# Kernel optimization log

Hardware: AMD Instinct MI355X
Metric: run time of the kernel (lower is better)

Reference implementation:

```python
import jax, jax.numpy as jnp
import numpy as np

T = 200000  # stack depth
V = 130     # vocab_size == input_dim
H = 512     # hid_dim
L = 2       # n_layers


def setup_inputs() -> dict:
    key = jax.random.key(0)
    ks = jax.random.split(key, 24)
    s = 0.05
    inp = {
        "input": jax.random.normal(ks[0], (1, 1, V), jnp.float32),
        "prev_Val": jax.random.normal(ks[1], (T, V), jnp.float32),
        "prev_stg": jax.random.uniform(ks[2], (T,), jnp.float32),
        "prev_read": jax.random.normal(ks[3], (V,), jnp.float32),
        "prev_h": jax.random.normal(ks[4], (L, 1, H), jnp.float32) * 0.1,
        "prev_c": jax.random.normal(ks[5], (L, 1, H), jnp.float32) * 0.1,
        # LSTM layer 0 (pytorch layout: W_ih (4H, in), W_hh (4H, H), gates i,f,g,o)
        "W_ih0": jax.random.normal(ks[6], (4 * H, V), jnp.float32) * s,
        "W_hh0": jax.random.normal(ks[7], (4 * H, H), jnp.float32) * s,
        "b_ih0": jax.random.normal(ks[8], (4 * H,), jnp.float32) * s,
        "b_hh0": jax.random.normal(ks[9], (4 * H,), jnp.float32) * s,
        # LSTM layer 1
        "W_ih1": jax.random.normal(ks[10], (4 * H, H), jnp.float32) * s,
        "W_hh1": jax.random.normal(ks[11], (4 * H, H), jnp.float32) * s,
        "b_ih1": jax.random.normal(ks[12], (4 * H,), jnp.float32) * s,
        "b_hh1": jax.random.normal(ks[13], (4 * H,), jnp.float32) * s,
        # gate heads (original inits these to zeros; random here to exercise math)
        "Wd": jax.random.normal(ks[14], (H,), jnp.float32) * s,
        "Bd": jax.random.normal(ks[15], (), jnp.float32) * s,
        "Wu": jax.random.normal(ks[16], (H,), jnp.float32) * s,
        "Bu": jax.random.normal(ks[17], (), jnp.float32) * s,
        "Wv": jax.random.normal(ks[18], (H, V), jnp.float32) * s,
        "Bv": jax.random.normal(ks[19], (V,), jnp.float32) * s,
        "Wo": jax.random.normal(ks[20], (H, H), jnp.float32) * s,
        "Bo": jax.random.normal(ks[21], (H,), jnp.float32) * s,
    }
    return inp


def _lstm_cell(x, h, c, Wih, Whh, bih, bhh):
    # x: (1, in), h/c: (1, H)
    g = x @ Wih.T + h @ Whh.T + bih + bhh  # (1, 4H)
    i, f, gg, o = jnp.split(g, 4, axis=-1)
    c2 = jax.nn.sigmoid(f) * c + jax.nn.sigmoid(i) * jnp.tanh(gg)
    h2 = jax.nn.sigmoid(o) * jnp.tanh(c2)
    return h2, c2


def reference(input, prev_Val, prev_stg, prev_read, prev_h, prev_c,
              W_ih0, W_hh0, b_ih0, b_hh0, W_ih1, W_hh1, b_ih1, b_hh1,
              Wd, Bd, Wu, Bu, Wv, Bv, Wo, Bo):
    x = (input + prev_read)[0]  # (1, V), seq_len == 1, batch == 1
    h1, c1 = _lstm_cell(x, prev_h[0], prev_c[0], W_ih0, W_hh0, b_ih0, b_hh0)
    h2, c2 = _lstm_cell(h1, prev_h[1], prev_c[1], W_ih1, W_hh1, b_ih1, b_hh1)
    output = h2  # (1, H)

    dt = jax.nn.sigmoid(output @ Wd + Bd)[0]      # scalar push strength
    ut = jax.nn.sigmoid(output @ Wu + Bu)[0]      # scalar pop strength
    vt = jnp.tanh(output @ Wv + Bv)               # (1, V) pushed value
    ot = jnp.tanh(output @ Wo + Bo)               # (1, H) controller output

    Val = jnp.concatenate([prev_Val, vt], axis=0)  # (T+1, V)

    # pop pass (top -> bottom): stg[i] = max(0, prev_stg[i] - max(0, ut)); ut -= stg[i]
    def pop_step(u, s):
        sn = jnp.maximum(0.0, s - jnp.maximum(0.0, u))
        return u - sn, sn
    _, stg_popped = jax.lax.scan(pop_step, ut, prev_stg, reverse=True)
    stg = jnp.concatenate([stg_popped, dt[None]])  # (T+1,)

    # read pass (top -> bottom): coef = min(stg[i], max(0, read)); read -= stg[i]
    def read_step(r, s):
        coef = jnp.minimum(s, jnp.maximum(0.0, r))
        return r - s, coef
    _, coefs = jax.lax.scan(read_step, jnp.asarray(1.0, stg.dtype), stg, reverse=True)
    rt = coefs @ Val  # (V,)

    h_new = jnp.stack([h1, h2])  # (L, 1, H)
    c_new = jnp.stack([c1, c2])
    return ot, Val, stg, rt, h_new, c_new
```

## Files before the change

kernel.cpp:

```cpp
#include <hip/hip_runtime.h>

#define T_DEPTH 200000
#define V_DIM   130
#define H_DIM   512

#define OT_OFF   0
#define VAL_OFF  512
#define STG_OFF  26000642
#define RT_OFF   26200643
#define HN_OFF   26200773
#define CN_OFF   26201797

#define WS_G0     0
#define WS_H1     2048
#define WS_C1     2560
#define WS_G1     3072
#define WS_H2     5120
#define WS_C2     5632
#define WS_VTACC  6144
#define WS_OTACC  6274
#define WS_DTUT   6786
#define WS_VT     6788
#define WS_TOTAL  6918

static __device__ __forceinline__ float sigmoidf(float x) {
    return 1.0f / (1.0f + expf(-x));
}

__global__ void k_bulk(const float4* __restrict__ val_in,
                       const float2* __restrict__ stg_in,
                       float* __restrict__ out) {
    const int NV4 = (T_DEPTH * V_DIM) / 4;
    const int NS2 = T_DEPTH / 2;
    const int NT  = NV4 + NS2;
    float4* __restrict__ val_out = reinterpret_cast<float4*>(out + VAL_OFF);
    float2* __restrict__ stg_out = reinterpret_cast<float2*>(out + STG_OFF);
    int stride = gridDim.x * blockDim.x;
    for (int u = blockIdx.x * blockDim.x + threadIdx.x; u < NT; u += stride) {
        if (u < NV4) {
            val_out[u] = val_in[u];
        } else {
            int s = u - NV4;
            stg_out[s] = stg_in[s];
        }
    }
}

__global__ void k_g0(const float* __restrict__ Wih, const float* __restrict__ Whh,
                     const float* __restrict__ bih, const float* __restrict__ bhh,
                     const float* __restrict__ inp, const float* __restrict__ prd,
                     const float* __restrict__ h0, float* __restrict__ g) {
    int wave = threadIdx.x >> 6, lane = threadIdx.x & 63;
    int row = blockIdx.x * 4 + wave;
    const float* wr = Wih + row * V_DIM;
    const float* wh = Whh + row * H_DIM;
    float p = 0.f;
    for (int c = lane; c < V_DIM; c += 64) p += wr[c] * (inp[c] + prd[c]);
    for (int k = lane; k < H_DIM; k += 64) p += wh[k] * h0[k];
    for (int off = 32; off; off >>= 1) p += __shfl_down(p, off, 64);
    if (lane == 0) g[row] = p + bih[row] + bhh[row];
}

__global__ void k_g1(const float* __restrict__ Wih, const float* __restrict__ Whh,
                     const float* __restrict__ bih, const float* __restrict__ bhh,
                     const float* __restrict__ h1, const float* __restrict__ hprev,
                     float* __restrict__ g) {
    int wave = threadIdx.x >> 6, lane = threadIdx.x & 63;
    int row = blockIdx.x * 4 + wave;
    const float* wr = Wih + row * H_DIM;
    const float* wh = Whh + row * H_DIM;
    float p = 0.f;
    for (int k = lane; k < H_DIM; k += 64) p += wr[k] * h1[k] + wh[k] * hprev[k];
    for (int off = 32; off; off >>= 1) p += __shfl_down(p, off, 64);
    if (lane == 0) g[row] = p + bih[row] + bhh[row];
}

__global__ void k_cell(const float* __restrict__ g, const float* __restrict__ cprev,
                       float* __restrict__ h, float* __restrict__ c,
                       float* __restrict__ h_out, float* __restrict__ c_out) {
    int j = threadIdx.x;
    float ig = sigmoidf(g[j]);
    float fg = sigmoidf(g[H_DIM + j]);
    float gg = tanhf(g[2 * H_DIM + j]);
    float og = sigmoidf(g[3 * H_DIM + j]);
    float cn = fg * cprev[j] + ig * gg;
    float hn = og * tanhf(cn);
    h[j] = hn; c[j] = cn;
    h_out[j] = hn;
    c_out[j] = cn;
}

__global__ void k_heads(const float* __restrict__ h2, const float* __restrict__ Wv,
                        const float* __restrict__ Wo, float* __restrict__ vt_acc,
                        float* __restrict__ ot_acc) {
    int t = threadIdx.x;
    int b = blockIdx.x;
    float a0 = 0.f, a1 = 0.f, av = 0.f;
    for (int kk = 0; kk < 16; ++kk) {
        int k = b * 16 + kk;
        float hv = h2[k];
        a0 += hv * Wo[k * H_DIM + t];
        a1 += hv * Wo[k * H_DIM + t + 256];
        if (t < V_DIM) av += hv * Wv[k * V_DIM + t];
    }
    atomicAdd(&ot_acc[t], a0);
    atomicAdd(&ot_acc[t + 256], a1);
    if (t < V_DIM) atomicAdd(&vt_acc[t], av);
}

__global__ void k_hfin(const float* __restrict__ h2,
                       const float* __restrict__ Wd, const float* __restrict__ Bd,
                       const float* __restrict__ Wu, const float* __restrict__ Bu,
                       const float* __restrict__ Bv, const float* __restrict__ Bo,
                       const float* __restrict__ vt_acc, const float* __restrict__ ot_acc,
                       float* __restrict__ dtut, float* __restrict__ vt,
                       float* __restrict__ out) {
    __shared__ float sd[H_DIM], su[H_DIM];
    int t = threadIdx.x;
    sd[t] = h2[t] * Wd[t];
    su[t] = h2[t] * Wu[t];
    __syncthreads();
    for (int s = 256; s; s >>= 1) {
        if (t < s) { sd[t] += sd[t + s]; su[t] += su[t + s]; }
        __syncthreads();
    }
    if (t == 0) {
        float dt = sigmoidf(sd[0] + Bd[0]);
        float ut = sigmoidf(su[0] + Bu[0]);
        dtut[0] = dt; dtut[1] = ut;
        out[STG_OFF + T_DEPTH] = dt;
    }
    float ot = tanhf(ot_acc[t] + Bo[t]);
    out[OT_OFF + t] = ot;
    if (t < V_DIM) {
        float v = tanhf(vt_acc[t] + Bv[t]);
        vt[t] = v;
        out[VAL_OFF + T_DEPTH * V_DIM + t] = v;
    }
}

__global__ void k_top(const float* __restrict__ prev_stg, const float* __restrict__ prev_val,
                      const float* __restrict__ dtut, const float* __restrict__ vt,
                      float* __restrict__ out) {
    int t = threadIdx.x;
    float dt = dtut[0];
    float u  = dtut[1];
    float r  = 1.0f;
    float acc = 0.f;
    {
        float coef = fminf(dt, fmaxf(0.f, r));
        if (t < V_DIM) acc += coef * vt[t];
        r -= dt;
    }
    for (int i = T_DEPTH - 1; i >= 0; --i) {
        bool pop_active = (u > 0.f);
        if (!pop_active && r <= 0.f) break;
        float s  = prev_stg[i];
        float sn = fmaxf(0.f, s - fmaxf(0.f, u));
        u -= sn;
        if (pop_active && t == 0) out[STG_OFF + i] = sn;
        float coef = fminf(sn, fmaxf(0.f, r));
        r -= sn;
        if (coef > 0.f && t < V_DIM) acc += coef * prev_val[i * V_DIM + t];
    }
    if (t < V_DIM) out[RT_OFF + t] = acc;
}

extern "C" void kernel_launch(void* const* d_in, const int* in_sizes, int n_in,
                              void* d_out, int out_size, void* d_ws, size_t ws_size,
                              hipStream_t stream) {
    (void)in_sizes; (void)n_in; (void)out_size; (void)ws_size;
    const float* input     = (const float*)d_in[0];
    const float* prev_Val  = (const float*)d_in[1];
    const float* prev_stg  = (const float*)d_in[2];
    const float* prev_read = (const float*)d_in[3];
    const float* prev_h    = (const float*)d_in[4];
    const float* prev_c    = (const float*)d_in[5];
    const float* W_ih0 = (const float*)d_in[6];
    const float* W_hh0 = (const float*)d_in[7];
    const float* b_ih0 = (const float*)d_in[8];
    const float* b_hh0 = (const float*)d_in[9];
    const float* W_ih1 = (const float*)d_in[10];
    const float* W_hh1 = (const float*)d_in[11];
    const float* b_ih1 = (const float*)d_in[12];
    const float* b_hh1 = (const float*)d_in[13];
    const float* Wd = (const float*)d_in[14];
    const float* Bd = (const float*)d_in[15];
    const float* Wu = (const float*)d_in[16];
    const float* Bu = (const float*)d_in[17];
    const float* Wv = (const float*)d_in[18];
    const float* Bv = (const float*)d_in[19];
    const float* Wo = (const float*)d_in[20];
    const float* Bo = (const float*)d_in[21];

    float* out = (float*)d_out;
    float* ws  = (float*)d_ws;

    hipMemsetAsync(d_ws, 0, WS_TOTAL * sizeof(float), stream);

    k_bulk<<<4096, 256, 0, stream>>>((const float4*)prev_Val, (const float2*)prev_stg, out);

    k_g0<<<512, 256, 0, stream>>>(W_ih0, W_hh0, b_ih0, b_hh0, input, prev_read,
                                  prev_h, ws + WS_G0);
    k_cell<<<1, 512, 0, stream>>>(ws + WS_G0, prev_c, ws + WS_H1, ws + WS_C1,
                                  out + HN_OFF, out + CN_OFF);
    k_g1<<<512, 256, 0, stream>>>(W_ih1, W_hh1, b_ih1, b_hh1, ws + WS_H1,
                                  prev_h + H_DIM, ws + WS_G1);
    k_cell<<<1, 512, 0, stream>>>(ws + WS_G1, prev_c + H_DIM, ws + WS_H2, ws + WS_C2,
                                  out + HN_OFF + H_DIM, out + CN_OFF + H_DIM);

    k_heads<<<32, 256, 0, stream>>>(ws + WS_H2, Wv, Wo, ws + WS_VTACC, ws + WS_OTACC);
    k_hfin<<<1, 512, 0, stream>>>(ws + WS_H2, Wd, Bd, Wu, Bu, Bv, Bo,
                                  ws + WS_VTACC, ws + WS_OTACC,
                                  ws + WS_DTUT, ws + WS_VT, out);

    k_top<<<1, 192, 0, stream>>>(prev_stg, prev_Val, ws + WS_DTUT, ws + WS_VT, out);
}
```

Measured before the change: 275.6 us.

## Overlap bulk stack copy with LSTM chain by fusing work into four kernels

```diff
diff --git a/kernel.cpp b/kernel.cpp
--- a/kernel.cpp
+++ b/kernel.cpp
@@ -11,208 +11,237 @@
 #define HN_OFF   26200773
 #define CN_OFF   26201797
 
-#define WS_G0     0
-#define WS_H1     2048
-#define WS_C1     2560
-#define WS_G1     3072
-#define WS_H2     5120
-#define WS_C2     5632
-#define WS_VTACC  6144
-#define WS_OTACC  6274
-#define WS_DTUT   6786
-#define WS_VT     6788
-#define WS_TOTAL  6918
-
-static __device__ __forceinline__ float sigmoidf(float x) {
-    return 1.0f / (1.0f + expf(-x));
-}
-
-__global__ void k_bulk(const float4* __restrict__ val_in,
-                       const float2* __restrict__ stg_in,
-                       float* __restrict__ out) {
-    const int NV4 = (T_DEPTH * V_DIM) / 4;
-    const int NS2 = T_DEPTH / 2;
-    const int NT  = NV4 + NS2;
-    float4* __restrict__ val_out = reinterpret_cast<float4*>(out + VAL_OFF);
-    float2* __restrict__ stg_out = reinterpret_cast<float2*>(out + STG_OFF);
-    int stride = gridDim.x * blockDim.x;
-    for (int u = blockIdx.x * blockDim.x + threadIdx.x; u < NT; u += stride) {
-        if (u < NV4) {
-            val_out[u] = val_in[u];
-        } else {
-            int s = u - NV4;
-            stg_out[s] = stg_in[s];
-        }
-    }
-}
-
-__global__ void k_g0(const float* __restrict__ Wih, const float* __restrict__ Whh,
-                     const float* __restrict__ bih, const float* __restrict__ bhh,
-                     const float* __restrict__ inp, const float* __restrict__ prd,
-                     const float* __restrict__ h0, float* __restrict__ g) {
-    int wave = threadIdx.x >> 6, lane = threadIdx.x & 63;
-    int row = blockIdx.x * 4 + wave;
-    const float* wr = Wih + row * V_DIM;
+#define NV4 6500000
+#define NS2 100000
+#define A1  1625000
+#define A2  3250000
+#define A3  4875000
+#define MVB 128
+#define CPB 1536
+
+typedef float f32x4 __attribute__((ext_vector_type(4)));
+typedef float f32x2 __attribute__((ext_vector_type(2)));
+
+static __device__ __forceinline__ float sigmoidf_(float x) {
+  return 1.0f / (1.0f + expf(-x));
+}
+
+static __device__ __forceinline__ void copy_val4(const f32x4* __restrict__ vin,
+                                                 f32x4* __restrict__ vout,
+                                                 int lo, int hi, int w, int S) {
+  int u = lo + w;
+  for (; u + 3 * S < hi; u += 4 * S) {
+    f32x4 a = __builtin_nontemporal_load(vin + u);
+    f32x4 b = __builtin_nontemporal_load(vin + u + S);
+    f32x4 c = __builtin_nontemporal_load(vin + u + 2 * S);
+    f32x4 d = __builtin_nontemporal_load(vin + u + 3 * S);
+    __builtin_nontemporal_store(a, vout + u);
+    __builtin_nontemporal_store(b, vout + u + S);
+    __builtin_nontemporal_store(c, vout + u + 2 * S);
+    __builtin_nontemporal_store(d, vout + u + 3 * S);
+  }
+  for (; u < hi; u += S) {
+    f32x4 a = __builtin_nontemporal_load(vin + u);
+    __builtin_nontemporal_store(a, vout + u);
+  }
+}
+
+static __device__ __forceinline__ void lstm_unit(
+    const float* __restrict__ Wih, int in_dim,
+    const float* __restrict__ x_a, const float* __restrict__ x_b,
+    const float* __restrict__ Whh, const float* __restrict__ hprev,
+    const float* __restrict__ bih, const float* __restrict__ bhh,
+    const float* __restrict__ cprev, int j, int lane,
+    float* __restrict__ h_out, float* __restrict__ c_out) {
+  float pg[4];
+#pragma unroll
+  for (int q = 0; q < 4; ++q) {
+    int row = q * H_DIM + j;
+    const float* wr = Wih + row * in_dim;
     const float* wh = Whh + row * H_DIM;
-    float p = 0.f;
-    for (int c = lane; c < V_DIM; c += 64) p += wr[c] * (inp[c] + prd[c]);
-    for (int k = lane; k < H_DIM; k += 64) p += wh[k] * h0[k];
-    for (int off = 32; off; off >>= 1) p += __shfl_down(p, off, 64);
-    if (lane == 0) g[row] = p + bih[row] + bhh[row];
-}
-
-__global__ void k_g1(const float* __restrict__ Wih, const float* __restrict__ Whh,
-                     const float* __restrict__ bih, const float* __restrict__ bhh,
-                     const float* __restrict__ h1, const float* __restrict__ hprev,
-                     float* __restrict__ g) {
-    int wave = threadIdx.x >> 6, lane = threadIdx.x & 63;
-    int row = blockIdx.x * 4 + wave;
-    const float* wr = Wih + row * H_DIM;
-    const float* wh = Whh + row * H_DIM;
-    float p = 0.f;
-    for (int k = lane; k < H_DIM; k += 64) p += wr[k] * h1[k] + wh[k] * hprev[k];
-    for (int off = 32; off; off >>= 1) p += __shfl_down(p, off, 64);
-    if (lane == 0) g[row] = p + bih[row] + bhh[row];
-}
-
-__global__ void k_cell(const float* __restrict__ g, const float* __restrict__ cprev,
-                       float* __restrict__ h, float* __restrict__ c,
-                       float* __restrict__ h_out, float* __restrict__ c_out) {
-    int j = threadIdx.x;
-    float ig = sigmoidf(g[j]);
-    float fg = sigmoidf(g[H_DIM + j]);
-    float gg = tanhf(g[2 * H_DIM + j]);
-    float og = sigmoidf(g[3 * H_DIM + j]);
+    float acc = 0.f;
+    if (x_b) {
+      for (int c = lane; c < in_dim; c += 64) acc += wr[c] * (x_a[c] + x_b[c]);
+    } else {
+      for (int c = lane; c < in_dim; c += 64) acc += wr[c] * x_a[c];
+    }
+    for (int k = lane; k < H_DIM; k += 64) acc += wh[k] * hprev[k];
+    for (int off = 32; off; off >>= 1) acc += __shfl_down(acc, off, 64);
+    pg[q] = acc;
+  }
+  if (lane == 0) {
+    float ig = sigmoidf_(pg[0] + bih[j] + bhh[j]);
+    float fg = sigmoidf_(pg[1] + bih[H_DIM + j] + bhh[H_DIM + j]);
+    float gg = tanhf(pg[2] + bih[2 * H_DIM + j] + bhh[2 * H_DIM + j]);
+    float og = sigmoidf_(pg[3] + bih[3 * H_DIM + j] + bhh[3 * H_DIM + j]);
     float cn = fg * cprev[j] + ig * gg;
     float hn = og * tanhf(cn);
-    h[j] = hn; c[j] = cn;
     h_out[j] = hn;
     c_out[j] = cn;
-}
-
-__global__ void k_heads(const float* __restrict__ h2, const float* __restrict__ Wv,
-                        const float* __restrict__ Wo, float* __restrict__ vt_acc,
-                        float* __restrict__ ot_acc) {
-    int t = threadIdx.x;
-    int b = blockIdx.x;
-    float a0 = 0.f, a1 = 0.f, av = 0.f;
-    for (int kk = 0; kk < 16; ++kk) {
-        int k = b * 16 + kk;
-        float hv = h2[k];
-        a0 += hv * Wo[k * H_DIM + t];
-        a1 += hv * Wo[k * H_DIM + t + 256];
-        if (t < V_DIM) av += hv * Wv[k * V_DIM + t];
-    }
-    atomicAdd(&ot_acc[t], a0);
-    atomicAdd(&ot_acc[t + 256], a1);
-    if (t < V_DIM) atomicAdd(&vt_acc[t], av);
-}
-
-__global__ void k_hfin(const float* __restrict__ h2,
-                       const float* __restrict__ Wd, const float* __restrict__ Bd,
-                       const float* __restrict__ Wu, const float* __restrict__ Bu,
-                       const float* __restrict__ Bv, const float* __restrict__ Bo,
-                       const float* __restrict__ vt_acc, const float* __restrict__ ot_acc,
-                       float* __restrict__ dtut, float* __restrict__ vt,
+  }
+}
+
+__global__ void k1_l0(const float* __restrict__ Wih, const float* __restrict__ Whh,
+                      const float* __restrict__ bih, const float* __restrict__ bhh,
+                      const float* __restrict__ inp, const float* __restrict__ prd,
+                      const float* __restrict__ hprev, const float* __restrict__ cprev,
+                      const f32x4* __restrict__ vin, const f32x2* __restrict__ sin2,
+                      float* __restrict__ out) {
+  int bid = blockIdx.x, tid = threadIdx.x;
+  if (bid < MVB) {
+    lstm_unit(Wih, V_DIM, inp, prd, Whh, hprev, bih, bhh, cprev,
+              bid * 4 + (tid >> 6), tid & 63, out + HN_OFF, out + CN_OFF);
+  } else {
+    int w = (bid - MVB) * 256 + tid;
+    int S = (gridDim.x - MVB) * 256;
+    f32x2* __restrict__ sout = reinterpret_cast<f32x2*>(out + STG_OFF);
+    for (int u = w; u < NS2; u += S) {
+      f32x2 sv = __builtin_nontemporal_load(sin2 + u);
+      __builtin_nontemporal_store(sv, sout + u);
+    }
+    copy_val4(vin, reinterpret_cast<f32x4*>(out + VAL_OFF), 0, A1, w, S);
+  }
+}
+
+__global__ void k2_l1(const float* __restrict__ Wih, const float* __restrict__ Whh,
+                      const float* __restrict__ bih, const float* __restrict__ bhh,
+                      const float* __restrict__ hprev, const float* __restrict__ cprev,
+                      const f32x4* __restrict__ vin, float* __restrict__ out) {
+  int bid = blockIdx.x, tid = threadIdx.x;
+  if (bid < MVB) {
+    lstm_unit(Wih, H_DIM, out + HN_OFF, nullptr, Whh, hprev, bih, bhh, cprev,
+              bid * 4 + (tid >> 6), tid & 63,
+              out + HN_OFF + H_DIM, out + CN_OFF + H_DIM);
+  } else {
+    int w = (bid - MVB) * 256 + tid;
+    int S = (gridDim.x - MVB) * 256;
+    copy_val4(vin, reinterpret_cast<f32x4*>(out + VAL_OFF), A1, A2, w, S);
+  }
+}
+
+__global__ void k3_heads(const float* __restrict__ Wv, const float* __restrict__ Bv,
+                         const float* __restrict__ Wo, const float* __restrict__ Bo,
+                         const float* __restrict__ Wd, const float* __restrict__ Bd,
+                         const float* __restrict__ Wu, const float* __restrict__ Bu,
+                         const f32x4* __restrict__ vin, float* __restrict__ ws,
+                         float* __restrict__ out) {
+  int bid = blockIdx.x, tid = threadIdx.x;
+  const float* h2 = out + HN_OFF + H_DIM;
+  if (bid < 2) {
+    int t = bid * 256 + tid;
+    float a0 = 0.f, a1 = 0.f, a2 = 0.f, a3 = 0.f;
+    for (int k = 0; k < H_DIM; k += 4) {
+      a0 += h2[k]     * Wo[k * H_DIM + t];
+      a1 += h2[k + 1] * Wo[(k + 1) * H_DIM + t];
+      a2 += h2[k + 2] * Wo[(k + 2) * H_DIM + t];
+      a3 += h2[k + 3] * Wo[(k + 3) * H_DIM + t];
+    }
+    out[OT_OFF + t] = tanhf(((a0 + a1) + (a2 + a3)) + Bo[t]);
+  } else if (bid == 2) {
+    if (tid < V_DIM) {
+      float a0 = 0.f, a1 = 0.f, a2 = 0.f, a3 = 0.f;
+      for (int k = 0; k < H_DIM; k += 4) {
+        a0 += h2[k]     * Wv[k * V_DIM + tid];
+        a1 += h2[k + 1] * Wv[(k + 1) * V_DIM + tid];
+        a2 += h2[k + 2] * Wv[(k + 2) * V_DIM + tid];
+        a3 += h2[k + 3] * Wv[(k + 3) * V_DIM + tid];
+      }
+      out[VAL_OFF + T_DEPTH * V_DIM + tid] = tanhf(((a0 + a1) + (a2 + a3)) + Bv[tid]);
+    }
+  } else if (bid == 3) {
+    int wid = tid >> 6, lane = tid & 63;
+    if (wid < 2) {
+      const float* wv = (wid == 0) ? Wd : Wu;
+      float acc = 0.f;
+      for (int k = lane; k < H_DIM; k += 64) acc += h2[k] * wv[k];
+      for (int off = 32; off; off >>= 1) acc += __shfl_down(acc, off, 64);
+      if (lane == 0) {
+        if (wid == 0) {
+          float dt = sigmoidf_(acc + Bd[0]);
+          ws[0] = dt;
+          out[STG_OFF + T_DEPTH] = dt;
+        } else {
+          ws[1] = sigmoidf_(acc + Bu[0]);
+        }
+      }
+    }
+  } else {
+    int w = (bid - 4) * 256 + tid;
+    int S = (gridDim.x - 4) * 256;
+    copy_val4(vin, reinterpret_cast<f32x4*>(out + VAL_OFF), A2, A3, w, S);
+  }
+}
+
+__global__ void k4_top(const float* __restrict__ prev_stg, const float* __restrict__ prev_val,
+                       const float* __restrict__ ws, const f32x4* __restrict__ vin,
                        float* __restrict__ out) {
-    __shared__ float sd[H_DIM], su[H_DIM];
-    int t = threadIdx.x;
-    sd[t] = h2[t] * Wd[t];
-    su[t] = h2[t] * Wu[t];
-    __syncthreads();
-    for (int s = 256; s; s >>= 1) {
-        if (t < s) { sd[t] += sd[t + s]; su[t] += su[t + s]; }
-        __syncthreads();
-    }
-    if (t == 0) {
-        float dt = sigmoidf(sd[0] + Bd[0]);
-        float ut = sigmoidf(su[0] + Bu[0]);
-        dtut[0] = dt; dtut[1] = ut;
-        out[STG_OFF + T_DEPTH] = dt;
-    }
-    float ot = tanhf(ot_acc[t] + Bo[t]);
-    out[OT_OFF + t] = ot;
-    if (t < V_DIM) {
-        float v = tanhf(vt_acc[t] + Bv[t]);
-        vt[t] = v;
-        out[VAL_OFF + T_DEPTH * V_DIM + t] = v;
-    }
-}
-
-__global__ void k_top(const float* __restrict__ prev_stg, const float* __restrict__ prev_val,
-                      const float* __restrict__ dtut, const float* __restrict__ vt,
-                      float* __restrict__ out) {
-    int t = threadIdx.x;
-    float dt = dtut[0];
-    float u  = dtut[1];
+  int bid = blockIdx.x, t = threadIdx.x;
+  if (bid == 0) {
+    float dt = ws[0];
+    float u  = ws[1];
     float r  = 1.0f;
     float acc = 0.f;
     {
-        float coef = fminf(dt, fmaxf(0.f, r));
-        if (t < V_DIM) acc += coef * vt[t];
-        r -= dt;
+      float coef = fminf(dt, fmaxf(0.f, r));
+      if (t < V_DIM) acc += coef * out[VAL_OFF + T_DEPTH * V_DIM + t];
+      r -= dt;
     }
     for (int i = T_DEPTH - 1; i >= 0; --i) {
-        bool pop_active = (u > 0.f);
-        if (!pop_active && r <= 0.f) break;
-        float s  = prev_stg[i];
-        float sn = fmaxf(0.f, s - fmaxf(0.f, u));
-        u -= sn;
-        if (pop_active && t == 0) out[STG_OFF + i] = sn;
-        float coef = fminf(sn, fmaxf(0.f, r));
-        r -= sn;
-        if (coef > 0.f && t < V_DIM) acc += coef * prev_val[i * V_DIM + t];
+      bool pop_active = (u > 0.f);
+      if (!pop_active && r <= 0.f) break;
+      float s  = prev_stg[i];
+      float sn = fmaxf(0.f, s - fmaxf(0.f, u));
+      u -= sn;
+      if (pop_active && t == 0) out[STG_OFF + i] = sn;
+      float coef = fminf(sn, fmaxf(0.f, r));
+      r -= sn;
+      if (coef > 0.f && t < V_DIM) acc += coef * prev_val[i * V_DIM + t];
     }
     if (t < V_DIM) out[RT_OFF + t] = acc;
+  } else {
+    int w = (bid - 1) * 256 + t;
+    int S = (gridDim.x - 1) * 256;
+    copy_val4(vin, reinterpret_cast<f32x4*>(out + VAL_OFF), A3, NV4, w, S);
+  }
 }
 
 extern "C" void kernel_launch(void* const* d_in, const int* in_sizes, int n_in,
                               void* d_out, int out_size, void* d_ws, size_t ws_size,
                               hipStream_t stream) {
-    (void)in_sizes; (void)n_in; (void)out_size; (void)ws_size;
-    const float* input     = (const float*)d_in[0];
-    const float* prev_Val  = (const float*)d_in[1];
-    const float* prev_stg  = (const float*)d_in[2];
-    const float* prev_read = (const float*)d_in[3];
-    const float* prev_h    = (const float*)d_in[4];
-    const float* prev_c    = (const float*)d_in[5];
-    const float* W_ih0 = (const float*)d_in[6];
-    const float* W_hh0 = (const float*)d_in[7];
-    const float* b_ih0 = (const float*)d_in[8];
-    const float* b_hh0 = (const float*)d_in[9];
-    const float* W_ih1 = (const float*)d_in[10];
-    const float* W_hh1 = (const float*)d_in[11];
-    const float* b_ih1 = (const float*)d_in[12];
-    const float* b_hh1 = (const float*)d_in[13];
-    const float* Wd = (const float*)d_in[14];
-    const float* Bd = (const float*)d_in[15];
-    const float* Wu = (const float*)d_in[16];
-    const float* Bu = (const float*)d_in[17];
-    const float* Wv = (const float*)d_in[18];
-    const float* Bv = (const float*)d_in[19];
-    const float* Wo = (const float*)d_in[20];
-    const float* Bo = (const float*)d_in[21];
-
-    float* out = (float*)d_out;
-    float* ws  = (float*)d_ws;
-
-    hipMemsetAsync(d_ws, 0, WS_TOTAL * sizeof(float), stream);
-
-    k_bulk<<<4096, 256, 0, stream>>>((const float4*)prev_Val, (const float2*)prev_stg, out);
-
-    k_g0<<<512, 256, 0, stream>>>(W_ih0, W_hh0, b_ih0, b_hh0, input, prev_read,
-                                  prev_h, ws + WS_G0);
-    k_cell<<<1, 512, 0, stream>>>(ws + WS_G0, prev_c, ws + WS_H1, ws + WS_C1,
-                                  out + HN_OFF, out + CN_OFF);
-    k_g1<<<512, 256, 0, stream>>>(W_ih1, W_hh1, b_ih1, b_hh1, ws + WS_H1,
-                                  prev_h + H_DIM, ws + WS_G1);
-    k_cell<<<1, 512, 0, stream>>>(ws + WS_G1, prev_c + H_DIM, ws + WS_H2, ws + WS_C2,
-                                  out + HN_OFF + H_DIM, out + CN_OFF + H_DIM);
-
-    k_heads<<<32, 256, 0, stream>>>(ws + WS_H2, Wv, Wo, ws + WS_VTACC, ws + WS_OTACC);
-    k_hfin<<<1, 512, 0, stream>>>(ws + WS_H2, Wd, Bd, Wu, Bu, Bv, Bo,
-                                  ws + WS_VTACC, ws + WS_OTACC,
-                                  ws + WS_DTUT, ws + WS_VT, out);
-
-    k_top<<<1, 192, 0, stream>>>(prev_stg, prev_Val, ws + WS_DTUT, ws + WS_VT, out);
-}
+  (void)in_sizes; (void)n_in; (void)out_size; (void)ws_size;
+  const float* input     = (const float*)d_in[0];
+  const float* prev_Val  = (const float*)d_in[1];
+  const float* prev_stg  = (const float*)d_in[2];
+  const float* prev_read = (const float*)d_in[3];
+  const float* prev_h    = (const float*)d_in[4];
+  const float* prev_c    = (const float*)d_in[5];
+  const float* W_ih0 = (const float*)d_in[6];
+  const float* W_hh0 = (const float*)d_in[7];
+  const float* b_ih0 = (const float*)d_in[8];
+  const float* b_hh0 = (const float*)d_in[9];
+  const float* W_ih1 = (const float*)d_in[10];
+  const float* W_hh1 = (const float*)d_in[11];
+  const float* b_ih1 = (const float*)d_in[12];
+  const float* b_hh1 = (const float*)d_in[13];
+  const float* Wd = (const float*)d_in[14];
+  const float* Bd = (const float*)d_in[15];
+  const float* Wu = (const float*)d_in[16];
+  const float* Bu = (const float*)d_in[17];
+  const float* Wv = (const float*)d_in[18];
+  const float* Bv = (const float*)d_in[19];
+  const float* Wo = (const float*)d_in[20];
+  const float* Bo = (const float*)d_in[21];
+
+  float* out = (float*)d_out;
+  float* ws  = (float*)d_ws;
+
+  const f32x4* vin = (const f32x4*)prev_Val;
+  const f32x2* sin2 = (const f32x2*)prev_stg;
+
+  k1_l0<<<MVB + CPB, 256, 0, stream>>>(W_ih0, W_hh0, b_ih0, b_hh0, input, prev_read,
+                                       prev_h, prev_c, vin, sin2, out);
+  k2_l1<<<MVB + CPB, 256, 0, stream>>>(W_ih1, W_hh1, b_ih1, b_hh1,
+                                       prev_h + H_DIM, prev_c + H_DIM, vin, out);
+  k3_heads<<<4 + CPB, 256, 0, stream>>>(Wv, Bv, Wo, Bo, Wd, Bd, Wu, Bu, vin, ws, out);
+  k4_top<<<1 + CPB, 256, 0, stream>>>(prev_stg, prev_Val, ws, vin, out);
+}
```

Result: slower. 297.2 us (+7.9%).
